# Kernel optimization log

Hardware: AMD Instinct MI355X
Metric: run time of the kernel (lower is better)

Reference implementation:

```python
import jax, jax.numpy as jnp
import numpy as np

B_S, N_NODES, D_FEAT, N_HEADS, N_BLOCKS, AVG_DEG = 8, 4096, 128, 4, 32, 16
D_HID, N_CLASSES = 256, 16


def setup_inputs() -> dict:
    key = jax.random.key(0)
    ks = jax.random.split(key, 6)
    x = jax.random.normal(ks[0], (B_S, N_NODES, D_FEAT), jnp.float32)
    e_per = N_NODES * AVG_DEG
    src = jax.random.randint(ks[1], (B_S, e_per), 0, N_NODES)
    dst = jax.random.randint(ks[2], (B_S, e_per), 0, N_NODES)
    off = jnp.arange(B_S)[:, None] * N_NODES
    edge_index = jnp.stack([(src + off).reshape(-1), (dst + off).reshape(-1)], 0).astype(jnp.int32)
    W_rank = jax.random.normal(ks[3], (D_FEAT, N_HEADS), jnp.float32) / np.sqrt(D_FEAT)
    W1 = jax.random.normal(ks[4], (2 * D_FEAT, D_HID), jnp.float32) / np.sqrt(2.0 * D_FEAT)
    W_out = jax.random.normal(ks[5], (D_HID, N_CLASSES), jnp.float32) / np.sqrt(D_HID)
    return {"x": x, "W_rank": W_rank, "W1": W1, "W_out": W_out,
            "edge_index": edge_index, "j": N_BLOCKS}


def _forward(x, W_rank, W1, W_out, edge_index, j):
    b_s, n, d = x.shape
    h = W_rank.shape[1]
    k = n // j                      # block (subgraph) size; j*k == n
    Bp = h * b_s * j                # number of (head, graph, block) blocks
    src, dst = edge_index[0], edge_index[1]
    N = b_s * n
    x_flat = x.reshape(N, d)

    # GCN-normalized adjacency Ahat with self loops (selfloop=1)
    deg = jnp.ones(N, x.dtype).at[dst].add(1.0)
    w = jax.lax.rsqrt(deg[src] * deg[dst])

    def ahat_mv(v):  # Ahat @ v, v: [N, c]
        out = jnp.zeros_like(v).at[dst].add(w[:, None] * v[src])
        return out + v / deg[:, None]

    # app_adj: concat(x, Ahat @ x)
    x_appd = ahat_mv(x_flat)

    # ranking: linear scores + one propagation hop -> [b, h, n]
    scores = ahat_mv(x_flat @ W_rank)
    scores = scores.reshape(b_s, n, h).transpose(0, 2, 1)

    # perm_gen: full descending sort split into j blocks of k (sorted_idx [b,h,j,k])
    order = jnp.argsort(-scores, axis=-1)        # [b,h,n] node ids in rank order
    pos = jnp.argsort(order, axis=-1)            # inverse: node -> sorted slot
    sorted_scores = jnp.take_along_axis(scores, order, axis=-1)
    perm_val = jax.nn.sigmoid(sorted_scores).reshape(b_s, h, j, k)  # relaxed perm values
    sorted_blocks = order.reshape(b_s, h, j, k)
    # local target slot: rank of node id within each block (data-dependent perm)
    tgt = jnp.argsort(jnp.argsort(sorted_blocks, axis=-1), axis=-1)

    # gather features (with appended Ahat@x) into sorted block order
    feats = jnp.concatenate([x, x_appd.reshape(b_s, n, d)], -1)      # [b,n,2d]
    feats_sorted = feats[jnp.arange(b_s)[:, None, None], order]       # [b,h,n,2d]
    feats_in = feats_sorted.reshape(b_s, h, j, k, 2 * d).transpose(1, 0, 2, 3, 4).reshape(Bp, k, 2 * d)

    # edge masking per head: keep edges whose endpoints land in the same block,
    # remap to local slots -> dense block adjacency [Bp, k, k]
    b_e = src // n
    src_l, dst_l = src % n, dst % n
    heads = jnp.arange(h)
    pos_s = pos[b_e[:, None], heads[None, :], src_l[:, None]]   # [E,h]
    pos_d = pos[b_e[:, None], heads[None, :], dst_l[:, None]]
    blk_s, slot_s = pos_s // k, pos_s % k
    blk_d, slot_d = pos_d // k, pos_d % k
    keep = (blk_s == blk_d).astype(x.dtype)
    block_id = (heads[None, :] * b_s + b_e[:, None]) * j + blk_s  # (h,b,j) layout
    A = jnp.zeros((Bp, k, k), x.dtype).at[block_id, slot_s, slot_d].add(keep)

    # relaxed permutation matrix P[b', s, tgt_s] = v_s  (sub_size = 1)
    val_f = perm_val.transpose(1, 0, 2, 3).reshape(Bp, k)
    tgt_f = tgt.transpose(1, 0, 2, 3).reshape(Bp, k)
    P = jnp.zeros((Bp, k, k), x.dtype).at[
        jnp.arange(Bp)[:, None], jnp.arange(k)[None, :], tgt_f].set(val_f)

    # sparse_perm_2D: new_adj[tgt_s, tgt_t] += v_s * v_t * A[s, t]  ==  P^T A P
    A_perm = jnp.einsum('bsi,bst,btj->bij', P, A, P)
    X_perm = jnp.einsum('bsi,bsd->bid', P, feats_in)

    # cocn: one message-passing layer on permuted blocks + mean pool + head
    Hh = jax.nn.relu(jnp.einsum('bij,bjd->bid', A_perm, X_perm) @ W1)
    logits = Hh.mean(1) @ W_out                        # [Bp, C]
    logits = logits.reshape(h, b_s, j, -1).mean(0)     # head average -> [b, j, C]
    return jax.nn.log_softmax(logits, axis=-1)         # single-class task


def reference(x, W_rank, W1, W_out, edge_index, j):
    return _forward(x, W_rank, W1, W_out, edge_index, j)
```

## Files before the change

### kernel.cpp

```cpp
#include <hip/hip_runtime.h>
#include <cmath>

#define NB 8
#define NN 4096
#define DF 128
#define NH 4
#define NJ 32
#define NK 128
#define NTOT (NB*NN)
#define ETOT 524288
#define BPB (NH*NB*NJ)
#define DHID 256
#define NCLS 16
#define CAP_PB 96
#define CAP_BP 512

#define FP_SCALE 4194304.0
#define FP_INV   (1.0/4194304.0)

typedef short bf16x8 __attribute__((ext_vector_type(8)));
typedef float f32x4  __attribute__((ext_vector_type(4)));

__device__ __forceinline__ unsigned short f2bf(float f) {
    unsigned u = __float_as_uint(f);
    unsigned r = (u + 0x7FFFu + ((u >> 16) & 1u)) >> 16;
    return (unsigned short)r;
}
__device__ __forceinline__ float bf2f(unsigned short b) {
    unsigned u = ((unsigned)b) << 16;
    return __uint_as_float(u);
}

__device__ __forceinline__ unsigned long long make_key(float sc, int p) {
    unsigned u = __float_as_uint(sc);
    unsigned s = u ^ ((unsigned)((int)u >> 31) | 0x80000000u);
    return ((unsigned long long)(s ^ 0xFFFFFFFFu) << 12) | (unsigned)p;
}

__global__ void k0_init(int* deg_i, int* fill, int* fill2) {
    int t = blockIdx.x * blockDim.x + threadIdx.x;
    if (t < NTOT) { deg_i[t] = 0; fill2[t] = 0; }
    if (t < BPB) fill[t] = 0;
}

__global__ __launch_bounds__(256) void k1_deg_prep(const int* __restrict__ ei,
                                                   const float* __restrict__ x,
                                                   const float* __restrict__ W1,
                                                   const float* __restrict__ wr,
                                                   int* deg_i,
                                                   unsigned short* __restrict__ xbf,
                                                   unsigned short* __restrict__ w1t,
                                                   float* __restrict__ scores_pre) {
    int bid = blockIdx.x, tid = threadIdx.x;
    if (bid < 2048) {
        int e = (bid & 7) * 65536 + (bid >> 3) * 256 + tid;
        atomicAdd(&deg_i[ei[ETOT + e]], 1);
    } else if (bid < 4096) {
        int idx = (bid - 2048) * 256 + tid;
        const float* sp = x + (size_t)idx * 8;
        float4 lo = *(const float4*)sp;
        float4 hi = *(const float4*)(sp + 4);
        unsigned short u[8] = {f2bf(lo.x), f2bf(lo.y), f2bf(lo.z), f2bf(lo.w),
                               f2bf(hi.x), f2bf(hi.y), f2bf(hi.z), f2bf(hi.w)};
        *(bf16x8*)(xbf + (size_t)idx * 8) = *(bf16x8*)u;
    } else if (bid < 4352) {
        int t = (bid - 4096) * 256 + tid;
        int k = t >> 8, n = t & 255;
        w1t[n * 256 + k] = f2bf(W1[k * DHID + n]);
    } else {
        int t = (bid - 4352) * 256 + tid;
        int g = t >> 2, hh = t & 3;
        const float* xr = x + (size_t)g * DF;
        double acc = 0.0;
        for (int d0 = 0; d0 < DF; ++d0) acc += (double)xr[d0] * (double)wr[d0 * NH + hh];
        scores_pre[t] = (float)acc;
    }
}

__global__ __launch_bounds__(256) void k_prep2(const int* __restrict__ deg_i,
                                               float* __restrict__ rdeg,
                                               int* __restrict__ nbase) {
    int bid = blockIdx.x, tid = threadIdx.x;
    if (bid < 128) {
        int t = bid * 256 + tid;
        rdeg[t] = 1.0f / sqrtf((float)(1 + deg_i[t]));
        return;
    }
    __shared__ int part[256];
    int base0 = tid * 128;
    int s = 0;
    for (int i = 0; i < 128; ++i) s += deg_i[base0 + i];
    part[tid] = s;
    __syncthreads();
    for (int off = 1; off < 256; off <<= 1) {
        int v = (tid >= off) ? part[tid - off] : 0;
        __syncthreads();
        part[tid] += v;
        __syncthreads();
    }
    int running = (tid == 0) ? 0 : part[tid - 1];
    for (int i = 0; i < 128; ++i) {
        nbase[base0 + i] = running;
        running += deg_i[base0 + i];
    }
    if (tid == 255) nbase[NTOT] = running;
}

__global__ void k3c_fill_csr(const int* __restrict__ ei, const int* __restrict__ nbase,
                             int* fill2, int* __restrict__ csr_src) {
    int bid = blockIdx.x;
    int e = (bid & 7) * 65536 + (bid >> 3) * 256 + threadIdx.x;
    int s = ei[e], d = ei[ETOT + e];
    int slot = atomicAdd(&fill2[d], 1);
    csr_src[nbase[d] + slot] = s;
}

__global__ __launch_bounds__(256) void k4_gather(const int* __restrict__ csr_src,
                                                 const int* __restrict__ nbase,
                                                 const float* __restrict__ rdeg,
                                                 const float* __restrict__ x,
                                                 const unsigned short* __restrict__ xbf,
                                                 const float* __restrict__ scores_pre,
                                                 unsigned* __restrict__ xappbf,
                                                 int* __restrict__ iscore) {
    __shared__ unsigned long long nb[4][64];
    int bid = blockIdx.x;
    if (bid < 8192) {
        int swz = (bid & 7) * 1024 + (bid >> 3);
        int wid = threadIdx.x >> 6;
        int wv = swz * 4 + wid;
        int lane = threadIdx.x & 63;
        float rd = rdeg[wv];
        float2 v = ((const float2*)(x + (size_t)wv * DF))[lane];
        float acc0 = v.x * rd * rd, acc1 = v.y * rd * rd;
        int t0 = nbase[wv], t1 = nbase[wv + 1];
        int deg = t1 - t0;
        if (lane < deg && lane < 64) {
            int s = csr_src[t0 + lane];
            float w = rd * rdeg[s];
            nb[wid][lane] = ((unsigned long long)__float_as_uint(w) << 32)
                          | (unsigned)(s * DF);
        }
        int nfull = min(deg, 64);
#pragma unroll 4
        for (int t = 0; t < nfull; ++t) {
            unsigned long long e = nb[wid][t];
            float w = __uint_as_float((unsigned)(e >> 32));
            unsigned u = ((const unsigned*)(xbf + (e & 0xFFFFFFFFu)))[lane];
            acc0 = fmaf(w, bf2f((unsigned short)(u & 0xffff)), acc0);
            acc1 = fmaf(w, bf2f((unsigned short)(u >> 16)), acc1);
        }
        for (int t = t0 + 64; t < t1; ++t) {
            int s = csr_src[t];
            float w = rd * rdeg[s];
            unsigned u = ((const unsigned*)(xbf + (size_t)s * DF))[lane];
            acc0 = fmaf(w, bf2f((unsigned short)(u & 0xffff)), acc0);
            acc1 = fmaf(w, bf2f((unsigned short)(u >> 16)), acc1);
        }
        xappbf[(size_t)wv * 64 + lane] =
            (unsigned)f2bf(acc0) | ((unsigned)f2bf(acc1) << 16);
    } else {
        int t = (bid - 8192) * 256 + threadIdx.x;
        int d = t >> 2, hh = t & 3;
        float rdd = rdeg[d];
        int t0 = nbase[d], t1 = nbase[d + 1];
        int acc = 0;
        for (int e = t0; e < t1; ++e) {
            int s = csr_src[e];
            float w = rdeg[s] * rdd;
            double term = (double)(w * scores_pre[s * NH + hh]);
            acc += __double2int_rn(term * FP_SCALE);
        }
        iscore[t] = acc;
    }
}

__global__ __launch_bounds__(256) void kg5a(const unsigned short* __restrict__ xbf,
                                            const unsigned short* __restrict__ xappbf,
                                            const unsigned short* __restrict__ w1t,
                                            unsigned short* __restrict__ Gbf,
                                            const float* __restrict__ scores_pre,
                                            const int* __restrict__ iscore,
                                            const int* __restrict__ deg_i,
                                            unsigned long long* __restrict__ sorted64) {
    __shared__ __align__(16) unsigned char smem[32768];
    int bid = blockIdx.x, tid = threadIdx.x;
    if (bid < 512) {
        unsigned short* As = (unsigned short*)smem;
        unsigned short* Bs = (unsigned short*)(smem + 16384);
        int m0 = (bid >> 1) * 128, n0 = (bid & 1) * 128;
        int lane = tid & 63, wid = tid >> 6;
        int wr = wid >> 1, wc = wid & 1;
        f32x4 acc[4][4];
#pragma unroll
        for (int mi = 0; mi < 4; ++mi)
#pragma unroll
            for (int ni = 0; ni < 4; ++ni) acc[mi][ni] = f32x4{0.f, 0.f, 0.f, 0.f};
        for (int kk = 0; kk < 4; ++kk) {
            int k0 = kk * 64;
            const unsigned short* Asrc = (kk < 2) ? xbf : xappbf;
            int kbase = k0 & 127;
#pragma unroll
            for (int i = 0; i < 4; ++i) {
                int gi = tid + i * 256;
                int r = gi >> 3, c = gi & 7;
                int csrc = c ^ (r & 7);
                *(bf16x8*)&As[r * 64 + c * 8] =
                    *(const bf16x8*)(Asrc + (size_t)(m0 + r) * DF + kbase + csrc * 8);
            }
#pragma unroll
            for (int i = 0; i < 4; ++i) {
                int gi = tid + i * 256;
                int r = gi >> 3, c = gi & 7;
                int csrc = c ^ (r & 7);
                *(bf16x8*)&Bs[r * 64 + c * 8] =
                    *(const bf16x8*)(w1t + (size_t)(n0 + r) * 256 + k0 + csrc * 8);
            }
            __syncthreads();
#pragma unroll
            for (int ks = 0; ks < 2; ++ks) {
                bf16x8 af[4], bfr[4];
#pragma unroll
                for (int mi = 0; mi < 4; ++mi) {
                    int r = wr * 64 + mi * 16 + (lane & 15);
                    int gl = ks * 4 + (lane >> 4);
                    af[mi] = *(const bf16x8*)&As[r * 64 + (gl ^ (r & 7)) * 8];
                }
#pragma unroll
                for (int ni = 0; ni < 4; ++ni) {
                    int r = wc * 64 + ni * 16 + (lane & 15);
                    int gl = ks * 4 + (lane >> 4);
                    bfr[ni] = *(const bf16x8*)&Bs[r * 64 + (gl ^ (r & 7)) * 8];
                }
#pragma unroll
                for (int mi = 0; mi < 4; ++mi)
#pragma unroll
                    for (int ni = 0; ni < 4; ++ni)
                        acc[mi][ni] = __builtin_amdgcn_mfma_f32_16x16x32_bf16(
                            af[mi], bfr[ni], acc[mi][ni], 0, 0, 0);
            }
            __syncthreads();
        }
#pragma unroll
        for (int mi = 0; mi < 4; ++mi) {
            int rbase = m0 + wr * 64 + mi * 16 + (lane >> 4) * 4;
#pragma unroll
            for (int ni = 0; ni < 4; ++ni) {
                int col = n0 + wc * 64 + ni * 16 + (lane & 15);
#pragma unroll
                for (int j = 0; j < 4; ++j)
                    Gbf[(size_t)(rbase + j) * DHID + col] = f2bf(acc[mi][ni][j]);
            }
        }
        return;
    }
    unsigned long long* sk = (unsigned long long*)smem;
    int blk = bid - 512;
    int seg = blk >> 3, chunk = blk & 7;
    int b = seg >> 2, hh = seg & 3;
    for (int i = tid; i < 512; i += 256) {
        int p = chunk * 512 + i;
        int g = b * NN + p;
        float dg = (float)(1 + deg_i[g]);
        float sc = scores_pre[g * NH + hh] / dg + (float)((double)iscore[g * NH + hh] * FP_INV);
        sk[i] = make_key(sc, p);
    }
    __syncthreads();
    for (int size = 2; size <= 512; size <<= 1) {
        for (int stride = size >> 1; stride > 0; stride >>= 1) {
            for (int p = tid; p < 512; p += 256) {
                int q = p ^ stride;
                if (q > p) {
                    unsigned long long kp = sk[p], kq = sk[q];
                    bool before_qp = (kq < kp);
                    bool asc = ((p & size) == 0);
                    if (asc ? before_qp : !before_qp) { sk[p] = kq; sk[q] = kp; }
                }
            }
            __syncthreads();
        }
    }
    for (int i = tid; i < 512; i += 256)
        sorted64[seg * NN + chunk * 512 + i] = sk[i];
}

__global__ __launch_bounds__(256) void k5b_rank(const unsigned long long* __restrict__ sorted64,
                                                int* __restrict__ order, int* __restrict__ pos,
                                                float* __restrict__ val) {
    int t = blockIdx.x * 256 + threadIdx.x;
    int seg = t >> 12, i = t & 4095;
    int chunk = i >> 9, slot = i & 511;
    const unsigned long long* segp = sorted64 + (size_t)seg * NN;
    unsigned long long k = segp[chunk * 512 + slot];
    int rank = slot;
#pragma unroll
    for (int c = 0; c < 8; ++c) {
        if (c == chunk) continue;
        const unsigned long long* cp = segp + c * 512;
        int lo = 0, hi = 512;
        while (lo < hi) { int mid = (lo + hi) >> 1; lo = (cp[mid] < k) ? mid + 1 : lo; hi = (cp[mid] < k) ? hi : mid; }
        rank += lo;
    }
    int p = (int)(k & 4095u);
    pos[seg * NN + p] = rank;
    order[seg * NN + rank] = p;
    unsigned s = (unsigned)(k >> 12) ^ 0xFFFFFFFFu;
    unsigned u = s ^ (((int)s >= 0) ? 0xFFFFFFFFu : 0x80000000u);
    float sc = __uint_as_float(u);
    val[seg * NN + rank] = 1.0f / (1.0f + expf(-sc));
}

__global__ __launch_bounds__(256) void k56_tgt_bin(const int* __restrict__ order,
                                                   const int* __restrict__ ei,
                                                   const int* __restrict__ pos,
                                                   int* __restrict__ tgt,
                                                   int* fill, unsigned* __restrict__ elist) {
    __shared__ unsigned short pos_l[NN];
    __shared__ unsigned buf[NJ][CAP_PB];
    __shared__ int lcnt[NJ];
    __shared__ int gbase[NJ];
    int bid = blockIdx.x, tid = threadIdx.x;
    if (bid < 512) {
        int* o = (int*)pos_l;
        int base = bid * 256;
        o[tid] = order[base + tid];
        __syncthreads();
        int g0 = tid & ~127;
        int me = o[tid];
        int r = 0;
#pragma unroll 16
        for (int s2 = 0; s2 < 128; ++s2) r += (o[g0 + s2] < me) ? 1 : 0;
        tgt[base + tid] = r;
        return;
    }
    int blkid = bid - 512;
    int ph = blkid >> 3, part = blkid & 7;
    int b = ph >> 2, hh = ph & 3;
    for (int i = tid; i < NN; i += 256) pos_l[i] = (unsigned short)pos[ph * NN + i];
    if (tid < NJ) lcnt[tid] = 0;
    __syncthreads();
    int ebase = b * 65536 + part * 8192;
    for (int i = tid; i < 8192; i += 256) {
        int e = ebase + i;
        int s = ei[e], d = ei[ETOT + e];
        int ps = pos_l[s & 4095], pd = pos_l[d & 4095];
        if ((ps >> 7) == (pd >> 7)) {
            int blk = ps >> 7;
            int slot = atomicAdd(&lcnt[blk], 1);
            if (slot < CAP_PB)
                buf[blk][slot] = (unsigned)((ps & 127) | ((pd & 127) << 16));
        }
    }
    __syncthreads();
    if (tid < NJ) {
        int n = min(lcnt[tid], CAP_PB);
        lcnt[tid] = n;
        gbase[tid] = atomicAdd(&fill[((hh * NB + b) * NJ) + tid], n);
    }
    __syncthreads();
    for (int t = tid; t < NJ * CAP_PB; t += 256) {
        int blk = t / CAP_PB, i = t % CAP_PB;
        if (i < lcnt[blk]) {
            int g0 = gbase[blk] + i;
            if (g0 < CAP_BP) {
                int bpid = ((hh * NB + b) * NJ) + blk;
                elist[bpid * CAP_BP + g0] = buf[blk][i];
            }
        }
    }
}

__global__ __launch_bounds__(256) void k9_block(const unsigned short* __restrict__ Gbf,
                                                const int* __restrict__ order,
                                                const float* __restrict__ val,
                                                const int* __restrict__ tgt,
                                                const int* __restrict__ fill,
                                                const unsigned* __restrict__ elist,
                                                const float* __restrict__ Wo,
                                                float* __restrict__ logits_bp) {
    __shared__ float val_s[NK];
    __shared__ int   node_s[NK];
    __shared__ int   tgt_s[NK];
    __shared__ int   rcnt[NK];
    __shared__ int   rend[NK];
    __shared__ int   rfill[NK];
    __shared__ unsigned es_meta[CAP_BP];
    __shared__ float    es_coef[CAP_BP];
    __shared__ float hvec[DHID];
    int i0 = blockIdx.x;
    int xcd = i0 & 7, r0 = i0 >> 3;
    int hh = r0 >> 5, blk = r0 & 31, b = xcd;
    int bp = (hh * NB + b) * NJ + blk;
    int ph = (b << 2) | hh;
    int tid = threadIdx.x;
    if (tid < NK) {
        int p = blk * NK + tid;
        node_s[tid] = order[ph * NN + p];
        val_s[tid]  = val[ph * NN + p];
        tgt_s[tid]  = tgt[ph * NN + p];
        rcnt[tid] = 0; rfill[tid] = 0;
    }
    __syncthreads();
    int e0 = bp * CAP_BP;
    int ne = min(fill[bp], CAP_BP);
    for (int t = tid; t < ne; t += 256)
        atomicAdd(&rcnt[tgt_s[elist[e0 + t] & 0xffff]], 1);
    __syncthreads();
    if (tid < NK) rend[tid] = rcnt[tid];
    __syncthreads();
    for (int off = 1; off < NK; off <<= 1) {
        int v = 0;
        if (tid < NK && tid >= off) v = rend[tid - off];
        __syncthreads();
        if (tid < NK) rend[tid] += v;
        __syncthreads();
    }
    for (int t = tid; t < ne; t += 256) {
        unsigned ent = elist[e0 + t];
        int ss = ent & 0xffff, sd = ent >> 16;
        int row = tgt_s[ss];
        int slot = atomicAdd(&rfill[row], 1);
        int p0 = rend[row] - rcnt[row] + slot;
        es_meta[p0] = ((unsigned)row << 16) | (unsigned)node_s[sd];
        es_coef[p0] = val_s[ss] * val_s[sd] * val_s[sd];
    }
    __syncthreads();
    size_t gb = (size_t)b * NN * DHID + tid;
    float hsum = 0.f, m = 0.f;
    int prev = -1;
#pragma unroll 4
    for (int i = 0; i < ne; ++i) {
        unsigned md = es_meta[i];
        int row = (int)(md >> 16);
        float g = bf2f(Gbf[gb + (size_t)(md & 0xffffu) * DHID]);
        float c = es_coef[i];
        bool flush = (row != prev);
        hsum += flush ? fmaxf(m, 0.f) : 0.f;
        m = flush ? c * g : fmaf(c, g, m);
        prev = row;
    }
    hsum += fmaxf(m, 0.f);
    hvec[tid] = hsum * (1.0f / NK);
    __syncthreads();
    if (tid < NCLS) {
        float s = 0.f;
        for (int q = 0; q < DHID; ++q) s = fmaf(hvec[q], Wo[q * NCLS + tid], s);
        logits_bp[bp * NCLS + tid] = s;
    }
}

__global__ void k10_final(const float* __restrict__ logits_bp, float* __restrict__ out) {
    int t = threadIdx.x;
    int b = t >> 5, blk = t & 31;
    float v[NCLS];
#pragma unroll
    for (int c = 0; c < NCLS; ++c) {
        float s = 0.f;
        for (int hh = 0; hh < NH; ++hh)
            s += logits_bp[(((hh * NB + b) * NJ) + blk) * NCLS + c];
        v[c] = s * 0.25f;
    }
    float mx = v[0];
#pragma unroll
    for (int c = 1; c < NCLS; ++c) mx = fmaxf(mx, v[c]);
    float se = 0.f;
#pragma unroll
    for (int c = 0; c < NCLS; ++c) se += expf(v[c] - mx);
    float lse = logf(se);
#pragma unroll
    for (int c = 0; c < NCLS; ++c) out[t * NCLS + c] = v[c] - mx - lse;
}

extern "C" void kernel_launch(void* const* d_in, const int* in_sizes, int n_in,
                              void* d_out, int out_size, void* d_ws, size_t ws_size,
                              hipStream_t stream) {
    const float* x  = (const float*)d_in[0];
    const float* wr = (const float*)d_in[1];
    const float* W1 = (const float*)d_in[2];
    const float* Wo = (const float*)d_in[3];
    const int*   ei = (const int*)d_in[4];

    char* ws = (char*)d_ws;
    int*      deg_i      = (int*)(ws + 0);
    float*    rdeg       = (float*)(ws + 131072);
    float*    scores_pre = (float*)(ws + 262144);
    int*      iscore     = (int*)(ws + 786432);
    unsigned short* xbf  = (unsigned short*)(ws + 1310720);
    unsigned* xappbf     = (unsigned*)(ws + 9699328);
    unsigned short* Gbf  = (unsigned short*)(ws + 18087936);
    int*      order      = (int*)(ws + 51642368);
    int*      pos        = (int*)(ws + 52166656);
    int*      tgt        = (int*)(ws + 52690944);
    float*    val        = (float*)(ws + 53215232);
    int*      fill       = (int*)(ws + 53743616);
    int*      csr_src    = (int*)(ws + 53755904);
    unsigned short* w1t  = (unsigned short*)(ws + 55853056);
    unsigned* elist      = (unsigned*)(ws + 53755904);
    float*    logits_bp  = (float*)(ws + 62144512);
    int*      nbase      = (int*)(ws + 62210048);
    int*      fill2      = (int*)(ws + 62341184);
    unsigned long long* sorted64 = (unsigned long long*)(ws + 62472256);

    k0_init<<<128, 256, 0, stream>>>(deg_i, fill, fill2);
    k1_deg_prep<<<4864, 256, 0, stream>>>(ei, x, W1, wr, deg_i, xbf, w1t, scores_pre);
    k_prep2<<<129, 256, 0, stream>>>(deg_i, rdeg, nbase);
    k3c_fill_csr<<<2048, 256, 0, stream>>>(ei, nbase, fill2, csr_src);
    k4_gather<<<8704, 256, 0, stream>>>(csr_src, nbase, rdeg, x, xbf, scores_pre, xappbf, iscore);
    kg5a<<<768, 256, 0, stream>>>(xbf, (const unsigned short*)xappbf, w1t, Gbf,
                                  scores_pre, iscore, deg_i, sorted64);
    k5b_rank<<<512, 256, 0, stream>>>(sorted64, order, pos, val);
    k56_tgt_bin<<<768, 256, 0, stream>>>(order, ei, pos, tgt, fill, elist);
    k9_block<<<BPB, 256, 0, stream>>>(Gbf, order, val, tgt, fill, elist, Wo, logits_bp);
    k10_final<<<1, 256, 0, stream>>>(logits_bp, (float*)d_out);
}
```

Measured before the change: 183.8 us.

## Drop target-slot ranking; group block rows by source slot since pooling is permutation-invariant

After: 182.5 us. About the same (-0.7%).

```diff
diff --git a/kernel.cpp b/kernel.cpp
--- a/kernel.cpp
+++ b/kernel.cpp
@@ -310,32 +310,17 @@
     val[seg * NN + rank] = 1.0f / (1.0f + expf(-sc));
 }
 
-__global__ __launch_bounds__(256) void k56_tgt_bin(const int* __restrict__ order,
-                                                   const int* __restrict__ ei,
-                                                   const int* __restrict__ pos,
-                                                   int* __restrict__ tgt,
-                                                   int* fill, unsigned* __restrict__ elist) {
+__global__ __launch_bounds__(256) void k56_bin(const int* __restrict__ ei,
+                                               const int* __restrict__ pos,
+                                               int* fill, unsigned* __restrict__ elist) {
     __shared__ unsigned short pos_l[NN];
     __shared__ unsigned buf[NJ][CAP_PB];
     __shared__ int lcnt[NJ];
     __shared__ int gbase[NJ];
-    int bid = blockIdx.x, tid = threadIdx.x;
-    if (bid < 512) {
-        int* o = (int*)pos_l;
-        int base = bid * 256;
-        o[tid] = order[base + tid];
-        __syncthreads();
-        int g0 = tid & ~127;
-        int me = o[tid];
-        int r = 0;
-#pragma unroll 16
-        for (int s2 = 0; s2 < 128; ++s2) r += (o[g0 + s2] < me) ? 1 : 0;
-        tgt[base + tid] = r;
-        return;
-    }
-    int blkid = bid - 512;
+    int blkid = blockIdx.x;
     int ph = blkid >> 3, part = blkid & 7;
     int b = ph >> 2, hh = ph & 3;
+    int tid = threadIdx.x;
     for (int i = tid; i < NN; i += 256) pos_l[i] = (unsigned short)pos[ph * NN + i];
     if (tid < NJ) lcnt[tid] = 0;
     __syncthreads();
@@ -373,20 +358,20 @@
 __global__ __launch_bounds__(256) void k9_block(const unsigned short* __restrict__ Gbf,
                                                 const int* __restrict__ order,
                                                 const float* __restrict__ val,
-                                                const int* __restrict__ tgt,
                                                 const int* __restrict__ fill,
                                                 const unsigned* __restrict__ elist,
                                                 const float* __restrict__ Wo,
                                                 float* __restrict__ logits_bp) {
     __shared__ float val_s[NK];
     __shared__ int   node_s[NK];
-    __shared__ int   tgt_s[NK];
     __shared__ int   rcnt[NK];
     __shared__ int   rend[NK];
     __shared__ int   rfill[NK];
+    __shared__ unsigned el_s[CAP_BP];
     __shared__ unsigned es_meta[CAP_BP];
     __shared__ float    es_coef[CAP_BP];
     __shared__ float hvec[DHID];
+    __shared__ int scan_tot;
     int i0 = blockIdx.x;
     int xcd = i0 & 7, r0 = i0 >> 3;
     int hh = r0 >> 5, blk = r0 & 31, b = xcd;
@@ -397,31 +382,35 @@
         int p = blk * NK + tid;
         node_s[tid] = order[ph * NN + p];
         val_s[tid]  = val[ph * NN + p];
-        tgt_s[tid]  = tgt[ph * NN + p];
         rcnt[tid] = 0; rfill[tid] = 0;
     }
-    __syncthreads();
     int e0 = bp * CAP_BP;
     int ne = min(fill[bp], CAP_BP);
+    for (int t = tid; t < ne; t += 256) el_s[t] = elist[e0 + t];
+    __syncthreads();
     for (int t = tid; t < ne; t += 256)
-        atomicAdd(&rcnt[tgt_s[elist[e0 + t] & 0xffff]], 1);
-    __syncthreads();
-    if (tid < NK) rend[tid] = rcnt[tid];
-    __syncthreads();
-    for (int off = 1; off < NK; off <<= 1) {
-        int v = 0;
-        if (tid < NK && tid >= off) v = rend[tid - off];
-        __syncthreads();
-        if (tid < NK) rend[tid] += v;
-        __syncthreads();
-    }
+        atomicAdd(&rcnt[el_s[t] & 0xffff], 1);
+    __syncthreads();
+    int v = 0;
+    if (tid < NK) {
+        v = rcnt[tid];
+        int lane = tid & 63;
+#pragma unroll
+        for (int off = 1; off < 64; off <<= 1) {
+            int u = __shfl_up(v, off, 64);
+            v += (lane >= off) ? u : 0;
+        }
+        if (tid == 63) scan_tot = v;
+    }
+    __syncthreads();
+    if (tid < NK) rend[tid] = v + ((tid >= 64) ? scan_tot : 0);
+    __syncthreads();
     for (int t = tid; t < ne; t += 256) {
-        unsigned ent = elist[e0 + t];
+        unsigned ent = el_s[t];
         int ss = ent & 0xffff, sd = ent >> 16;
-        int row = tgt_s[ss];
-        int slot = atomicAdd(&rfill[row], 1);
-        int p0 = rend[row] - rcnt[row] + slot;
-        es_meta[p0] = ((unsigned)row << 16) | (unsigned)node_s[sd];
+        int slot = atomicAdd(&rfill[ss], 1);
+        int p0 = rend[ss] - rcnt[ss] + slot;
+        es_meta[p0] = ((unsigned)ss << 16) | (unsigned)node_s[sd];
         es_coef[p0] = val_s[ss] * val_s[sd] * val_s[sd];
     }
     __syncthreads();
@@ -490,7 +479,6 @@
     unsigned short* Gbf  = (unsigned short*)(ws + 18087936);
     int*      order      = (int*)(ws + 51642368);
     int*      pos        = (int*)(ws + 52166656);
-    int*      tgt        = (int*)(ws + 52690944);
     float*    val        = (float*)(ws + 53215232);
     int*      fill       = (int*)(ws + 53743616);
     int*      csr_src    = (int*)(ws + 53755904);
@@ -509,7 +497,7 @@
     kg5a<<<768, 256, 0, stream>>>(xbf, (const unsigned short*)xappbf, w1t, Gbf,
                                   scores_pre, iscore, deg_i, sorted64);
     k5b_rank<<<512, 256, 0, stream>>>(sorted64, order, pos, val);
-    k56_tgt_bin<<<768, 256, 0, stream>>>(order, ei, pos, tgt, fill, elist);
-    k9_block<<<BPB, 256, 0, stream>>>(Gbf, order, val, tgt, fill, elist, Wo, logits_bp);
+    k56_bin<<<256, 256, 0, stream>>>(ei, pos, fill, elist);
+    k9_block<<<BPB, 256, 0, stream>>>(Gbf, order, val, fill, elist, Wo, logits_bp);
     k10_final<<<1, 256, 0, stream>>>(logits_bp, (float*)d_out);
 }
```
